# Performance work log

Measured on AMD Instinct MI355X. Metric: run time of the kernel, lower is better.

Reference implementation:

```python
import jax, jax.numpy as jnp
import numpy as np

VOCAB, EMB, HID, FF, NCLS = 1000, 32, 32, 16, 7
T, B = 512, 512


def setup_inputs() -> dict:
    key = jax.random.key(0)
    ks = jax.random.split(key, 10)
    s = 1.0 / np.sqrt(HID)
    return {
        "x": jax.random.randint(ks[0], (T, B), 0, VOCAB, dtype=jnp.int64)
        if jax.config.jax_enable_x64 else jax.random.randint(ks[0], (T, B), 0, VOCAB, dtype=jnp.int32),
        "emb": jax.random.normal(ks[1], (VOCAB, EMB), dtype=jnp.float32),
        "W_ih": jax.random.uniform(ks[2], (4 * HID, EMB), minval=-s, maxval=s, dtype=jnp.float32),
        "W_hh": jax.random.uniform(ks[3], (4 * HID, HID), minval=-s, maxval=s, dtype=jnp.float32),
        "b_ih": jax.random.uniform(ks[4], (4 * HID,), minval=-s, maxval=s, dtype=jnp.float32),
        "b_hh": jax.random.uniform(ks[5], (4 * HID,), minval=-s, maxval=s, dtype=jnp.float32),
        "W1": jax.random.uniform(ks[6], (FF, HID), minval=-s, maxval=s, dtype=jnp.float32),
        "b1": jax.random.uniform(ks[7], (FF,), minval=-s, maxval=s, dtype=jnp.float32),
        "W2": jax.random.uniform(ks[8], (NCLS, FF), minval=-s, maxval=s, dtype=jnp.float32),
        "b2": jax.random.uniform(ks[9], (NCLS,), minval=-s, maxval=s, dtype=jnp.float32),
    }


def _lstm(xg, W_hh):
    # xg: (T, B, 4H) precomputed input-to-gate projections (incl. both biases)
    Bn = xg.shape[1]
    h0 = jnp.zeros((Bn, HID), xg.dtype)
    c0 = jnp.zeros((Bn, HID), xg.dtype)

    def step(carry, xg_t):
        h, c = carry
        g = xg_t + h @ W_hh.T  # (B, 4H)
        i, f, gg, o = jnp.split(g, 4, axis=-1)  # PyTorch gate order i,f,g,o
        i = jax.nn.sigmoid(i)
        f = jax.nn.sigmoid(f)
        gg = jnp.tanh(gg)
        o = jax.nn.sigmoid(o)
        c = f * c + i * gg
        h = o * jnp.tanh(c)
        return (h, c), h

    _, hs = jax.lax.scan(step, (h0, c0), xg)
    return hs  # (T, B, H)


def reference(x, emb, W_ih, W_hh, b_ih, b_hh, W1, b1, W2, b2):
    e = emb[x]  # (T, B, EMB) embedding lookup
    xg = jnp.einsum('tbe,ge->tbg', e, W_ih) + b_ih + b_hh  # (T, B, 4H)
    hs = _lstm(xg, W_hh)  # (T, B, H)
    z = jax.nn.relu(jnp.einsum('tbh,fh->tbf', hs, W1) + b1)  # (T, B, FF)
    logits = jnp.einsum('tbf,cf->tbc', z, W2) + b2  # (T, B, NCLS)
    # torch F.softmax with dim=None on a 3D tensor softmaxes over dim 0
    return jax.nn.softmax(logits, axis=0)
```

## Files before the change

kernel.cpp:

```cpp
#include <hip/hip_runtime.h>
#include <math.h>

#define TT    512
#define BB    512
#define HID   32
#define EMB   32
#define FFD   16
#define NCLS  7
#define VOCABN 1000

__device__ __forceinline__ float rl(float v, int k) {
    return __int_as_float(__builtin_amdgcn_readlane(__float_as_int(v), k));
}
__device__ __forceinline__ float fast_rcp(float x) {
#if defined(__has_builtin)
#if __has_builtin(__builtin_amdgcn_rcpf)
    return __builtin_amdgcn_rcpf(x);
#else
    return 1.0f / x;
#endif
#else
    return 1.0f / x;
#endif
}
__device__ __forceinline__ float sigf(float x) { return fast_rcp(1.0f + __expf(-x)); }
__device__ __forceinline__ float tanh_fast(float x) { return 2.0f * sigf(2.0f * x) - 1.0f; }

__global__ __launch_bounds__(64) void build_xg(
    const float* __restrict__ emb, const float* __restrict__ W_ih,
    const float* __restrict__ b_ih, const float* __restrict__ b_hh,
    float2* __restrict__ tab)
{
    const int v = blockIdx.x;
    const int j = threadIdx.x;
    const float* e  = emb + v * EMB;
    const float* w0 = W_ih + j * EMB;
    const float* w1 = W_ih + (j + 64) * EMB;
    float a0 = b_ih[j]      + b_hh[j];
    float a1 = b_ih[j + 64] + b_hh[j + 64];
    #pragma unroll
    for (int k = 0; k < EMB; ++k) {
        const float ek = e[k];
        a0 = fmaf(w0[k], ek, a0);
        a1 = fmaf(w1[k], ek, a1);
    }
    tab[v * 64 + j] = make_float2(a0, a1);
}

__global__ __launch_bounds__(64, 1) void lstm_rec(
    const int* __restrict__ x, const float2* __restrict__ tab,
    const float* __restrict__ W_hh, float* __restrict__ hsout)
{
    const int b  = blockIdx.x;
    const int j  = threadIdx.x;
    const int m  = j & 31;
    const bool lo = j < 32;

    __shared__ float sh[8 * HID];

    float whhA[HID], whhB[HID];
    #pragma unroll
    for (int k = 0; k < HID; k += 4) {
        float4 a;
        a = *(const float4*)(W_hh + j * HID + k);        whhA[k]=a.x; whhA[k+1]=a.y; whhA[k+2]=a.z; whhA[k+3]=a.w;
        a = *(const float4*)(W_hh + (j + 64) * HID + k); whhB[k]=a.x; whhB[k+1]=a.y; whhB[k+2]=a.z; whhB[k+3]=a.w;
    }

    float h = 0.f, c = 0.f;
    float* hrow0 = hsout + (size_t)b * TT * HID;

    int xc = x[2 * BB + b], xd = x[3 * BB + b];
    float2 xg  = tab[(size_t)x[b] * 64 + j];
    float2 xg1 = tab[(size_t)x[1 * BB + b] * 64 + j];

    for (int t8 = 0; t8 < TT / 8; ++t8) {
        #pragma unroll
        for (int u = 0; u < 8; ++u) {
            const int t = t8 * 8 + u;
            float2 xg2 = tab[(size_t)xc * 64 + j];
            const int tn = (t + 4 < TT) ? (t + 4) : (TT - 1);
            const int xnew = x[tn * BB + b];

            float hs[HID];
            #pragma unroll
            for (int k = 0; k < HID; ++k) hs[k] = rl(h, k);

            float p0 = xg.x, p1 = 0.f, q0 = xg.y, q1 = 0.f;
            #pragma unroll
            for (int k = 0; k < HID; k += 2) {
                p0 = fmaf(whhA[k],   hs[k],   p0); p1 = fmaf(whhA[k+1], hs[k+1], p1);
                q0 = fmaf(whhB[k],   hs[k],   q0); q1 = fmaf(whhB[k+1], hs[k+1], q1);
            }
            const float accA = p0 + p1, accB = q0 + q1;

            const float actA = sigf(accA);
            const float sB   = lo ? 2.0f * accB : accB;
            const float sgB  = sigf(sB);
            const float actB = lo ? 2.0f * sgB - 1.0f : sgB;
            const float oA = __shfl_xor(actA, 32);
            const float oB = __shfl_xor(actB, 32);
            const float gi = lo ? actA : oA;
            const float gf = lo ? oA   : actA;
            const float gg = lo ? actB : oB;
            const float go = lo ? oB   : actB;
            c = fmaf(gf, c, gi * gg);
            h = go * tanh_fast(c);

            if (lo) sh[u * HID + m] = h;
            xg = xg1; xg1 = xg2; xc = xd; xd = xnew;
        }
        const float4 v = *(const float4*)(sh + j * 4);
        *(float4*)(hrow0 + t8 * 8 * HID + j * 4) = v;
    }
}

__global__ __launch_bounds__(256) void ff_softmax(
    const float* __restrict__ hs,
    const float* __restrict__ W1, const float* __restrict__ b1,
    const float* __restrict__ W2, const float* __restrict__ b2,
    float* __restrict__ out)
{
    const int b    = blockIdx.x;
    const int tid  = threadIdx.x;
    const int lane = tid & 63, wv = tid >> 6;
    const int t0   = tid * 2;

    __shared__ float redM[4][NCLS];
    __shared__ float redS[4][NCLS];

    float4 hv[16];
    const float4* hb = (const float4*)(hs + ((size_t)b * TT + t0) * HID);
    #pragma unroll
    for (int q = 0; q < 16; ++q) hv[q] = hb[q];

    float lg[2][NCLS];
    #pragma unroll
    for (int r = 0; r < 2; ++r) {
        const float* hr = (const float*)(hv + 8 * r);
        float z[FFD];
        #pragma unroll
        for (int f = 0; f < FFD; ++f) {
            float a = b1[f];
            #pragma unroll
            for (int k = 0; k < HID; ++k) a = fmaf(W1[f * HID + k], hr[k], a);
            z[f] = fmaxf(a, 0.f);
        }
        #pragma unroll
        for (int cc = 0; cc < NCLS; ++cc) {
            float a = b2[cc];
            #pragma unroll
            for (int f = 0; f < FFD; ++f) a = fmaf(W2[cc * FFD + f], z[f], a);
            lg[r][cc] = a;
        }
    }

    float M[NCLS], S[NCLS];
    #pragma unroll
    for (int cc = 0; cc < NCLS; ++cc) {
        float mm = fmaxf(lg[0][cc], lg[1][cc]);
        #pragma unroll
        for (int off = 32; off; off >>= 1) mm = fmaxf(mm, __shfl_xor(mm, off));
        if (lane == 0) redM[wv][cc] = mm;
    }
    __syncthreads();
    #pragma unroll
    for (int cc = 0; cc < NCLS; ++cc)
        M[cc] = fmaxf(fmaxf(redM[0][cc], redM[1][cc]), fmaxf(redM[2][cc], redM[3][cc]));

    #pragma unroll
    for (int cc = 0; cc < NCLS; ++cc) {
        float ss = __expf(lg[0][cc] - M[cc]) + __expf(lg[1][cc] - M[cc]);
        #pragma unroll
        for (int off = 32; off; off >>= 1) ss += __shfl_xor(ss, off);
        if (lane == 0) redS[wv][cc] = ss;
    }
    __syncthreads();
    #pragma unroll
    for (int cc = 0; cc < NCLS; ++cc)
        S[cc] = (redS[0][cc] + redS[1][cc]) + (redS[2][cc] + redS[3][cc]);

    #pragma unroll
    for (int r = 0; r < 2; ++r) {
        float* o = out + ((size_t)(t0 + r) * BB + b) * NCLS;
        #pragma unroll
        for (int cc = 0; cc < NCLS; ++cc)
            o[cc] = __expf(lg[r][cc] - M[cc]) * fast_rcp(S[cc]);
    }
}

template <bool TAB>
__global__ __launch_bounds__(64) void lstm_all(
    const int* __restrict__ x, const float* __restrict__ emb,
    const float* __restrict__ W_ih, const float* __restrict__ W_hh,
    const float* __restrict__ b_ih, const float* __restrict__ b_hh,
    const float* __restrict__ W1, const float* __restrict__ b1,
    const float* __restrict__ W2, const float* __restrict__ b2,
    const float2* __restrict__ tab, float* __restrict__ out)
{
    const int b  = blockIdx.x;
    const int j  = threadIdx.x;
    const int m  = j & 31;
    const bool lo = j < 32;
    const int rA = j, rB = j + 64;

    float whhA[HID], whhB[HID];
    #pragma unroll
    for (int k = 0; k < HID; k += 4) {
        float4 a;
        a = *(const float4*)(W_hh + rA * HID + k); whhA[k]=a.x; whhA[k+1]=a.y; whhA[k+2]=a.z; whhA[k+3]=a.w;
        a = *(const float4*)(W_hh + rB * HID + k); whhB[k]=a.x; whhB[k+1]=a.y; whhB[k+2]=a.z; whhB[k+3]=a.w;
    }
    float wihA[HID], wihB[HID];
    float biasA = 0.f, biasB = 0.f;
    if constexpr (!TAB) {
        #pragma unroll
        for (int k = 0; k < HID; k += 4) {
            float4 a;
            a = *(const float4*)(W_ih + rA * HID + k); wihA[k]=a.x; wihA[k+1]=a.y; wihA[k+2]=a.z; wihA[k+3]=a.w;
            a = *(const float4*)(W_ih + rB * HID + k); wihB[k]=a.x; wihB[k+1]=a.y; wihB[k+2]=a.z; wihB[k+3]=a.w;
        }
        biasA = b_ih[rA] + b_hh[rA];
        biasB = b_ih[rB] + b_hh[rB];
    }
    const int f16 = j & 15;
    float w1r[HID];
    #pragma unroll
    for (int k = 0; k < HID; ++k) w1r[k] = W1[f16 * HID + k];
    const int cls = j & 7;
    const int c7  = (cls < NCLS) ? cls : 0;
    float w2r[FFD];
    #pragma unroll
    for (int f = 0; f < FFD; ++f) w2r[f] = W2[c7 * FFD + f];
    const float b1v = b1[f16];
    const float b2v = b2[c7];

    float h = 0.f, c = 0.f;
    float mrun = -3.0e38f, srun = 0.f;

    auto gates = [&](float accA, float accB) {
        const float actA = sigf(accA);
        const float sB   = lo ? 2.0f * accB : accB;
        const float sgB  = sigf(sB);
        const float actB = lo ? 2.0f * sgB - 1.0f : sgB;
        const float oA = __shfl_xor(actA, 32);
        const float oB = __shfl_xor(actB, 32);
        const float gi = lo ? actA : oA;
        const float gf = lo ? oA   : actA;
        const float gg = lo ? actB : oB;
        const float go = lo ? oB   : actB;
        c = fmaf(gf, c, gi * gg);
        h = go * tanh_fast(c);
    };

    auto ff_head = [&](int t_out, const float* hsv) {
        float z0 = b1v, z1 = 0.f;
        #pragma unroll
        for (int k = 0; k < HID; k += 2) {
            z0 = fmaf(w1r[k],     hsv[k],     z0);
            z1 = fmaf(w1r[k + 1], hsv[k + 1], z1);
        }
        const float z = fmaxf(z0 + z1, 0.0f);
        float lgv = b2v;
        #pragma unroll
        for (int f = 0; f < FFD; ++f) lgv = fmaf(w2r[f], rl(z, f), lgv);
        const float mn = fmaxf(mrun, lgv);
        srun = fmaf(srun, __expf(mrun - mn), __expf(lgv - mn));
        mrun = mn;
        if (j < NCLS) out[(t_out * BB + b) * NCLS + j] = lgv;
    };

    int xvn1 = x[1 * BB + b];
    int xvn2 = x[2 * BB + b];
    float2 xg = make_float2(0.f, 0.f);
    float eA = 0.f;
    if constexpr (TAB) xg = tab[(size_t)x[b] * 64 + j];
    else               eA = emb[x[b] * EMB + m];

    if constexpr (TAB) {
        gates(xg.x, xg.y);
    } else {
        float es[EMB];
        #pragma unroll
        for (int k = 0; k < EMB; ++k) es[k] = rl(eA, k);
        float p0 = biasA, p1 = 0.f, q0 = biasB, q1 = 0.f;
        #pragma unroll
        for (int k = 0; k < EMB; k += 2) {
            p0 = fmaf(wihA[k],   es[k],   p0); p1 = fmaf(wihA[k+1], es[k+1], p1);
            q0 = fmaf(wihB[k],   es[k],   q0); q1 = fmaf(wihB[k+1], es[k+1], q1);
        }
        gates(p0 + p1, q0 + q1);
    }
    if constexpr (TAB) xg = tab[(size_t)xvn1 * 64 + j];
    else               eA = emb[xvn1 * EMB + m];
    xvn1 = xvn2;
    xvn2 = x[3 * BB + b];

    for (int t = 1; t < TT; ++t) {
        float2 xg_n = make_float2(0.f, 0.f);
        float  e_n  = 0.f;
        if (t + 1 < TT) {
            if constexpr (TAB) xg_n = tab[(size_t)xvn1 * 64 + j];
            else               e_n  = emb[xvn1 * EMB + m];
        }
        const int xv_n3 = (t + 3 < TT) ? x[(t + 3) * BB + b] : 0;

        float hsv[HID];
        #pragma unroll
        for (int k = 0; k < HID; ++k) hsv[k] = rl(h, k);

        ff_head(t - 1, hsv);

        float p0, p1 = 0.f, q0, q1 = 0.f;
        if constexpr (TAB) { p0 = xg.x; q0 = xg.y; }
        else               { p0 = biasA; q0 = biasB; }
        if constexpr (!TAB) {
            float es[EMB];
            #pragma unroll
            for (int k = 0; k < EMB; ++k) es[k] = rl(eA, k);
            #pragma unroll
            for (int k = 0; k < EMB; k += 2) {
                p0 = fmaf(wihA[k],   es[k],   p0); p1 = fmaf(wihA[k+1], es[k+1], p1);
                q0 = fmaf(wihB[k],   es[k],   q0); q1 = fmaf(wihB[k+1], es[k+1], q1);
            }
        }
        #pragma unroll
        for (int k = 0; k < HID; k += 2) {
            p0 = fmaf(whhA[k],   hsv[k],   p0); p1 = fmaf(whhA[k+1], hsv[k+1], p1);
            q0 = fmaf(whhB[k],   hsv[k],   q0); q1 = fmaf(whhB[k+1], hsv[k+1], q1);
        }
        gates(p0 + p1, q0 + q1);

        xg = xg_n; eA = e_n; xvn1 = xvn2; xvn2 = xv_n3;
    }

    {
        float hsv[HID];
        #pragma unroll
        for (int k = 0; k < HID; ++k) hsv[k] = rl(h, k);
        ff_head(TT - 1, hsv);
    }

    #pragma unroll 1
    for (int cc = 0; cc < NCLS; ++cc) {
        const float mc = rl(mrun, cc);
        const float sc = rl(srun, cc);
        const float ic = 1.0f / sc;
        #pragma unroll
        for (int i = 0; i < TT / 64; ++i) {
            const int t = j + 64 * i;
            const int a = (t * BB + b) * NCLS + cc;
            out[a] = __expf(out[a] - mc) * ic;
        }
    }
}

extern "C" void kernel_launch(void* const* d_in, const int* in_sizes, int n_in,
                              void* d_out, int out_size, void* d_ws, size_t ws_size,
                              hipStream_t stream) {
    const int*   x   = (const int*)  d_in[0];
    const float* emb = (const float*)d_in[1];
    const float* Wih = (const float*)d_in[2];
    const float* Whh = (const float*)d_in[3];
    const float* bih = (const float*)d_in[4];
    const float* bhh = (const float*)d_in[5];
    const float* W1  = (const float*)d_in[6];
    const float* b1  = (const float*)d_in[7];
    const float* W2  = (const float*)d_in[8];
    const float* b2  = (const float*)d_in[9];
    float* out = (float*)d_out;

    const size_t tab_bytes = (size_t)VOCABN * 128 * sizeof(float);
    const size_t hs_off    = 524288;
    const size_t hs_bytes  = (size_t)BB * TT * HID * sizeof(float);
    if (ws_size >= hs_off + hs_bytes) {
        float2* tab = (float2*)d_ws;
        float*  hs  = (float*)((char*)d_ws + hs_off);
        build_xg<<<VOCABN, 64, 0, stream>>>(emb, Wih, bih, bhh, tab);
        lstm_rec<<<BB, 64, 0, stream>>>(x, tab, Whh, hs);
        ff_softmax<<<BB, 256, 0, stream>>>(hs, W1, b1, W2, b2, out);
    } else if (ws_size >= tab_bytes) {
        float2* tab = (float2*)d_ws;
        build_xg<<<VOCABN, 64, 0, stream>>>(emb, Wih, bih, bhh, tab);
        lstm_all<true><<<BB, 64, 0, stream>>>(x, emb, Wih, Whh, bih, bhh,
                                              W1, b1, W2, b2, tab, out);
    } else {
        lstm_all<false><<<BB, 64, 0, stream>>>(x, emb, Wih, Whh, bih, bhh,
                                               W1, b1, W2, b2, nullptr, out);
    }
}
```

Before: 293.4 us.

## Pack two batch rows per wavefront in LSTM recurrence with per-lane full gates

The recurrence kernel now processes two batch elements per 64-lane wavefront, with each lane computing all four gates for one hidden unit instead of splitting gates across lane halves. The input-gate table is rebuilt as float4 per hidden unit so one load fetches all four gate inputs. The per-step readlane broadcast of h becomes ds_bpermute and the cross-half shuffles are removed. The aim is to halve the number of workgroups, which on MI355X's 256 CUs fits in a single wave, at the cost of twice the FMAs per lane on the serial critical path and bpermute latency per step.

```diff
diff --git a/kernel.cpp b/kernel.cpp
--- a/kernel.cpp
+++ b/kernel.cpp
@@ -47,70 +47,107 @@
     tab[v * 64 + j] = make_float2(a0, a1);
 }
 
-__global__ __launch_bounds__(64, 1) void lstm_rec(
-    const int* __restrict__ x, const float2* __restrict__ tab,
+__global__ __launch_bounds__(64) void build_xg4(
+    const float* __restrict__ emb, const float* __restrict__ W_ih,
+    const float* __restrict__ b_ih, const float* __restrict__ b_hh,
+    float4* __restrict__ tab4)
+{
+    const int v = blockIdx.x;
+    const int j = threadIdx.x;
+    __shared__ float g[128];
+    const float* e  = emb + v * EMB;
+    const float* w0 = W_ih + j * EMB;
+    const float* w1 = W_ih + (j + 64) * EMB;
+    float a0 = b_ih[j]      + b_hh[j];
+    float a1 = b_ih[j + 64] + b_hh[j + 64];
+    #pragma unroll
+    for (int k = 0; k < EMB; ++k) {
+        const float ek = e[k];
+        a0 = fmaf(w0[k], ek, a0);
+        a1 = fmaf(w1[k], ek, a1);
+    }
+    g[j] = a0; g[j + 64] = a1;
+    __syncthreads();
+    if (j < 32)
+        tab4[v * 32 + j] = make_float4(g[j], g[j + 32], g[j + 64], g[j + 96]);
+}
+
+__global__ __launch_bounds__(64, 1) void lstm_rec2(
+    const int* __restrict__ x, const float4* __restrict__ tab4,
     const float* __restrict__ W_hh, float* __restrict__ hsout)
 {
-    const int b  = blockIdx.x;
-    const int j  = threadIdx.x;
-    const int m  = j & 31;
-    const bool lo = j < 32;
-
-    __shared__ float sh[8 * HID];
-
-    float whhA[HID], whhB[HID];
+    const int blk  = blockIdx.x;
+    const int lane = threadIdx.x;
+    const int m    = lane & 31;
+    const int b0   = 2 * blk;
+    const int base4 = (lane & 32) * 4;
+
+    __shared__ float sh[8 * 64];
+
+    float wI[HID], wF[HID], wG[HID], wO[HID];
     #pragma unroll
     for (int k = 0; k < HID; k += 4) {
-        float4 a;
-        a = *(const float4*)(W_hh + j * HID + k);        whhA[k]=a.x; whhA[k+1]=a.y; whhA[k+2]=a.z; whhA[k+3]=a.w;
-        a = *(const float4*)(W_hh + (j + 64) * HID + k); whhB[k]=a.x; whhB[k+1]=a.y; whhB[k+2]=a.z; whhB[k+3]=a.w;
+        *(float4*)&wI[k] = *(const float4*)(W_hh + (m     ) * HID + k);
+        *(float4*)&wF[k] = *(const float4*)(W_hh + (m + 32) * HID + k);
+        *(float4*)&wG[k] = *(const float4*)(W_hh + (m + 64) * HID + k);
+        *(float4*)&wO[k] = *(const float4*)(W_hh + (m + 96) * HID + k);
     }
 
     float h = 0.f, c = 0.f;
-    float* hrow0 = hsout + (size_t)b * TT * HID;
-
-    int xc = x[2 * BB + b], xd = x[3 * BB + b];
-    float2 xg  = tab[(size_t)x[b] * 64 + j];
-    float2 xg1 = tab[(size_t)x[1 * BB + b] * 64 + j];
+
+    auto tabload = [&](int v0, int v1) -> float4 {
+        const int v = (lane < 32) ? v0 : v1;
+        return tab4[v * 32 + m];
+    };
+
+    int2 xvA = *(const int2*)(x + 2 * BB + b0);
+    int2 xvB = *(const int2*)(x + 3 * BB + b0);
+    int2 xv0 = *(const int2*)(x + 0 * BB + b0);
+    int2 xv1 = *(const int2*)(x + 1 * BB + b0);
+    float4 xg  = tabload(xv0.x, xv0.y);
+    float4 xg1 = tabload(xv1.x, xv1.y);
 
     for (int t8 = 0; t8 < TT / 8; ++t8) {
         #pragma unroll
         for (int u = 0; u < 8; ++u) {
             const int t = t8 * 8 + u;
-            float2 xg2 = tab[(size_t)xc * 64 + j];
+            float4 xg2 = tabload(xvA.x, xvA.y);
             const int tn = (t + 4 < TT) ? (t + 4) : (TT - 1);
-            const int xnew = x[tn * BB + b];
-
+            const int2 xnew = *(const int2*)(x + tn * BB + b0);
+
+            const int hb = __float_as_int(h);
             float hs[HID];
             #pragma unroll
-            for (int k = 0; k < HID; ++k) hs[k] = rl(h, k);
-
-            float p0 = xg.x, p1 = 0.f, q0 = xg.y, q1 = 0.f;
+            for (int k = 0; k < HID; ++k)
+                hs[k] = __int_as_float(__builtin_amdgcn_ds_bpermute(base4 + 4 * k, hb));
+
+            float i0 = xg.x, i1 = 0.f, f0 = xg.y, f1 = 0.f;
+            float g0 = xg.z, g1 = 0.f, o0 = xg.w, o1 = 0.f;
             #pragma unroll
             for (int k = 0; k < HID; k += 2) {
-                p0 = fmaf(whhA[k],   hs[k],   p0); p1 = fmaf(whhA[k+1], hs[k+1], p1);
-                q0 = fmaf(whhB[k],   hs[k],   q0); q1 = fmaf(whhB[k+1], hs[k+1], q1);
+                i0 = fmaf(wI[k], hs[k], i0); i1 = fmaf(wI[k+1], hs[k+1], i1);
+                f0 = fmaf(wF[k], hs[k], f0); f1 = fmaf(wF[k+1], hs[k+1], f1);
+                g0 = fmaf(wG[k], hs[k], g0); g1 = fmaf(wG[k+1], hs[k+1], g1);
+                o0 = fmaf(wO[k], hs[k], o0); o1 = fmaf(wO[k+1], hs[k+1], o1);
             }
-            const float accA = p0 + p1, accB = q0 + q1;
-
-            const float actA = sigf(accA);
-            const float sB   = lo ? 2.0f * accB : accB;
-            const float sgB  = sigf(sB);
-            const float actB = lo ? 2.0f * sgB - 1.0f : sgB;
-            const float oA = __shfl_xor(actA, 32);
-            const float oB = __shfl_xor(actB, 32);
-            const float gi = lo ? actA : oA;
-            const float gf = lo ? oA   : actA;
-            const float gg = lo ? actB : oB;
-            const float go = lo ? oB   : actB;
+            const float gi = sigf(i0 + i1);
+            const float gf = sigf(f0 + f1);
+            const float gg = tanh_fast(g0 + g1);
+            const float go = sigf(o0 + o1);
             c = fmaf(gf, c, gi * gg);
             h = go * tanh_fast(c);
 
-            if (lo) sh[u * HID + m] = h;
-            xg = xg1; xg1 = xg2; xc = xd; xd = xnew;
-        }
-        const float4 v = *(const float4*)(sh + j * 4);
-        *(float4*)(hrow0 + t8 * 8 * HID + j * 4) = v;
+            sh[u * 64 + lane] = h;
+            xg = xg1; xg1 = xg2; xvA = xvB; xvB = xnew;
+        }
+        {
+            const int e  = lane * 4;
+            const int u  = e >> 5, k0 = e & 31;
+            const float4 v0 = *(const float4*)(sh + u * 64 + k0);
+            const float4 v1 = *(const float4*)(sh + u * 64 + 32 + k0);
+            *(float4*)(hsout + ((size_t)b0       * TT + t8 * 8) * HID + e) = v0;
+            *(float4*)(hsout + ((size_t)(b0 + 1) * TT + t8 * 8) * HID + e) = v1;
+        }
     }
 }
 
@@ -373,10 +410,10 @@
     const size_t hs_off    = 524288;
     const size_t hs_bytes  = (size_t)BB * TT * HID * sizeof(float);
     if (ws_size >= hs_off + hs_bytes) {
-        float2* tab = (float2*)d_ws;
-        float*  hs  = (float*)((char*)d_ws + hs_off);
-        build_xg<<<VOCABN, 64, 0, stream>>>(emb, Wih, bih, bhh, tab);
-        lstm_rec<<<BB, 64, 0, stream>>>(x, tab, Whh, hs);
+        float4* tab4 = (float4*)d_ws;
+        float*  hs   = (float*)((char*)d_ws + hs_off);
+        build_xg4<<<VOCABN, 64, 0, stream>>>(emb, Wih, bih, bhh, tab4);
+        lstm_rec2<<<BB / 2, 64, 0, stream>>>(x, tab4, Whh, hs);
         ff_softmax<<<BB, 256, 0, stream>>>(hs, W1, b1, W2, b2, out);
     } else if (ws_size >= tab_bytes) {
         float2* tab = (float2*)d_ws;
```

Result: slower. 373.5 us (+27.3%).

## Process two batch sequences per wavefront in LSTM recurrence for ILP

Applied to the files above, without the earlier changes.

Each 64-thread block now runs the recurrence for two batch elements at once, interleaving their matvec FMAs and gate computations, and launches half as many blocks. The goal is to hide the latency of the serial per-step dependency chain (readlane, FMA, transcendental) by giving the wavefront two independent chains, and to drop to 256 blocks, which fits the CU count better. The cost is more registers and double the work per step on each wave, and the loss of parallelism if the CUs were not already saturated.

```diff
diff --git a/kernel.cpp b/kernel.cpp
--- a/kernel.cpp
+++ b/kernel.cpp
@@ -51,12 +51,13 @@
     const int* __restrict__ x, const float2* __restrict__ tab,
     const float* __restrict__ W_hh, float* __restrict__ hsout)
 {
-    const int b  = blockIdx.x;
-    const int j  = threadIdx.x;
-    const int m  = j & 31;
+    const int blk = blockIdx.x;
+    const int b0  = 2 * blk;
+    const int j   = threadIdx.x;
+    const int m   = j & 31;
     const bool lo = j < 32;
 
-    __shared__ float sh[8 * HID];
+    __shared__ float sh[2][8 * HID];
 
     float whhA[HID], whhB[HID];
     #pragma unroll
@@ -66,51 +67,64 @@
         a = *(const float4*)(W_hh + (j + 64) * HID + k); whhB[k]=a.x; whhB[k+1]=a.y; whhB[k+2]=a.z; whhB[k+3]=a.w;
     }
 
-    float h = 0.f, c = 0.f;
-    float* hrow0 = hsout + (size_t)b * TT * HID;
-
-    int xc = x[2 * BB + b], xd = x[3 * BB + b];
-    float2 xg  = tab[(size_t)x[b] * 64 + j];
-    float2 xg1 = tab[(size_t)x[1 * BB + b] * 64 + j];
+    float h0 = 0.f, c0 = 0.f, h1 = 0.f, c1 = 0.f;
+
+    auto gates = [&](float accA, float accB, float& c, float& h) {
+        const float actA = sigf(accA);
+        const float sB   = lo ? 2.0f * accB : accB;
+        const float sgB  = sigf(sB);
+        const float actB = lo ? 2.0f * sgB - 1.0f : sgB;
+        const float oA = __shfl_xor(actA, 32);
+        const float oB = __shfl_xor(actB, 32);
+        const float gi = lo ? actA : oA;
+        const float gf = lo ? oA   : actA;
+        const float gg = lo ? actB : oB;
+        const float go = lo ? oB   : actB;
+        c = fmaf(gf, c, gi * gg);
+        h = go * tanh_fast(c);
+    };
+
+    int2 xc = *(const int2*)(x + 2 * BB + b0);
+    int2 xd = *(const int2*)(x + 3 * BB + b0);
+    const int2 xv0 = *(const int2*)(x + 0 * BB + b0);
+    const int2 xv1 = *(const int2*)(x + 1 * BB + b0);
+    float2 xgA  = tab[(size_t)xv0.x * 64 + j];
+    float2 xgB  = tab[(size_t)xv0.y * 64 + j];
+    float2 xgA1 = tab[(size_t)xv1.x * 64 + j];
+    float2 xgB1 = tab[(size_t)xv1.y * 64 + j];
 
     for (int t8 = 0; t8 < TT / 8; ++t8) {
         #pragma unroll
         for (int u = 0; u < 8; ++u) {
             const int t = t8 * 8 + u;
-            float2 xg2 = tab[(size_t)xc * 64 + j];
+            float2 xgA2 = tab[(size_t)xc.x * 64 + j];
+            float2 xgB2 = tab[(size_t)xc.y * 64 + j];
             const int tn = (t + 4 < TT) ? (t + 4) : (TT - 1);
-            const int xnew = x[tn * BB + b];
-
-            float hs[HID];
-            #pragma unroll
-            for (int k = 0; k < HID; ++k) hs[k] = rl(h, k);
-
-            float p0 = xg.x, p1 = 0.f, q0 = xg.y, q1 = 0.f;
+            const int2 xnew = *(const int2*)(x + tn * BB + b0);
+
+            float p0A = xgA.x, p1A = 0.f, q0A = xgA.y, q1A = 0.f;
+            float p0B = xgB.x, p1B = 0.f, q0B = xgB.y, q1B = 0.f;
             #pragma unroll
             for (int k = 0; k < HID; k += 2) {
-                p0 = fmaf(whhA[k],   hs[k],   p0); p1 = fmaf(whhA[k+1], hs[k+1], p1);
-                q0 = fmaf(whhB[k],   hs[k],   q0); q1 = fmaf(whhB[k+1], hs[k+1], q1);
+                const float h0a = rl(h0, k),     h1a = rl(h1, k);
+                const float h0b = rl(h0, k + 1), h1b = rl(h1, k + 1);
+                p0A = fmaf(whhA[k],   h0a, p0A); q0A = fmaf(whhB[k],   h0a, q0A);
+                p0B = fmaf(whhA[k],   h1a, p0B); q0B = fmaf(whhB[k],   h1a, q0B);
+                p1A = fmaf(whhA[k+1], h0b, p1A); q1A = fmaf(whhB[k+1], h0b, q1A);
+                p1B = fmaf(whhA[k+1], h1b, p1B); q1B = fmaf(whhB[k+1], h1b, q1B);
             }
-            const float accA = p0 + p1, accB = q0 + q1;
-
-            const float actA = sigf(accA);
-            const float sB   = lo ? 2.0f * accB : accB;
-            const float sgB  = sigf(sB);
-            const float actB = lo ? 2.0f * sgB - 1.0f : sgB;
-            const float oA = __shfl_xor(actA, 32);
-            const float oB = __shfl_xor(actB, 32);
-            const float gi = lo ? actA : oA;
-            const float gf = lo ? oA   : actA;
-            const float gg = lo ? actB : oB;
-            const float go = lo ? oB   : actB;
-            c = fmaf(gf, c, gi * gg);
-            h = go * tanh_fast(c);
-
-            if (lo) sh[u * HID + m] = h;
-            xg = xg1; xg1 = xg2; xc = xd; xd = xnew;
-        }
-        const float4 v = *(const float4*)(sh + j * 4);
-        *(float4*)(hrow0 + t8 * 8 * HID + j * 4) = v;
+            gates(p0A + p1A, q0A + q1A, c0, h0);
+            gates(p0B + p1B, q0B + q1B, c1, h1);
+
+            if (lo) { sh[0][u * HID + m] = h0; sh[1][u * HID + m] = h1; }
+            xgA = xgA1; xgA1 = xgA2;
+            xgB = xgB1; xgB1 = xgB2;
+            xc = xd; xd = xnew;
+        }
+        const float4 v0 = *(const float4*)(&sh[0][j * 4]);
+        const float4 v1 = *(const float4*)(&sh[1][j * 4]);
+        *(float4*)(hsout + ((size_t)b0       * TT + t8 * 8) * HID + j * 4) = v0;
+        *(float4*)(hsout + ((size_t)(b0 + 1) * TT + t8 * 8) * HID + j * 4) = v1;
     }
 }
 
@@ -376,7 +390,7 @@
         float2* tab = (float2*)d_ws;
         float*  hs  = (float*)((char*)d_ws + hs_off);
         build_xg<<<VOCABN, 64, 0, stream>>>(emb, Wih, bih, bhh, tab);
-        lstm_rec<<<BB, 64, 0, stream>>>(x, tab, Whh, hs);
+        lstm_rec<<<BB / 2, 64, 0, stream>>>(x, tab, Whh, hs);
         ff_softmax<<<BB, 256, 0, stream>>>(hs, W1, b1, W2, b2, out);
     } else if (ws_size >= tab_bytes) {
         float2* tab = (float2*)d_ws;
```

Measured after the change: 389.7 us. 32.8% more time.
